# Performance work log

Measured on AMD Instinct MI355X. Metric: run time of the kernel, lower is better.

Reference implementation:

```python
import jax, jax.numpy as jnp
import numpy as np

DIM = 1024
HEADS = 16
DIM_HEAD = 64
B = 4
N = 2048
INNER = HEADS * DIM_HEAD
SCALE = DIM_HEAD ** -0.5
NEG = -1e9


def setup_inputs() -> dict:
    key = jax.random.key(0)
    k1, k2, k3 = jax.random.split(key, 3)
    x = jax.random.normal(k1, (B, N, DIM), dtype=jnp.float32)
    w_qkv = jax.random.normal(k2, (DIM, 3 * INNER), dtype=jnp.float32) * (DIM ** -0.5)
    w_out = jax.random.normal(k3, (INNER, DIM), dtype=jnp.float32) * (INNER ** -0.5)
    b_out = jnp.zeros((DIM,), dtype=jnp.float32)
    return {"x": x, "w_qkv": w_qkv, "w_out": w_out, "b_out": b_out}


def reference(x, w_qkv, w_out, b_out):
    b, n, _ = x.shape
    qkv = x @ w_qkv  # [b, n, 3*inner]
    q, k, v = jnp.split(qkv, 3, axis=-1)
    # [b, n, inner] -> [b, h, n, d]
    split_heads = lambda t: t.reshape(b, n, HEADS, DIM_HEAD).transpose(0, 2, 1, 3)
    q, k, v = split_heads(q), split_heads(k), split_heads(v)
    dots = jnp.einsum('bhid,bhjd->bhij', q, k) * SCALE
    causal = jnp.tril(jnp.ones((n, n), dtype=bool))  # mask[i,j]=1 for j<=i
    dots = jnp.where(causal, dots, NEG)
    attn = jax.nn.softmax(dots, axis=-1)
    out = jnp.einsum('bhij,bhjd->bhid', attn, v)
    out = out.transpose(0, 2, 1, 3).reshape(b, n, INNER)
    return out @ w_out + b_out
```

## Files before the change

### kernel.cpp

```cpp
#include <hip/hip_runtime.h>

typedef unsigned short u16;
typedef __attribute__((ext_vector_type(8))) short short8;
typedef __attribute__((ext_vector_type(4))) float f32x4;

#define MFMA_BF16(a, b, c) __builtin_amdgcn_mfma_f32_16x16x32_bf16((a), (b), (c), 0, 0, 0)

__device__ __forceinline__ void gl2lds16(const u16* g, u16* l) {
  __builtin_amdgcn_global_load_lds(
      (const __attribute__((address_space(1))) unsigned int*)g,
      (__attribute__((address_space(3))) unsigned int*)l, 16, 0, 0);
}

__device__ __forceinline__ u16 f2bf(float f) {
  union { float f; unsigned u; } v; v.f = f;
  unsigned r = v.u + 0x7fffu + ((v.u >> 16) & 1u);
  return (u16)(r >> 16);
}

__global__ void fill_one_f32(float* p, int n) {
  int i = blockIdx.x * blockDim.x + threadIdx.x;
  if (i < n) p[i] = 1.0f;
}

__global__ void prep_k(const float* __restrict__ x, u16* __restrict__ Xb,
                       const float* __restrict__ w_qkv, u16* __restrict__ wqkvT,
                       const float* __restrict__ w_out, u16* __restrict__ woutT) {
  __shared__ float tile[32][33];
  const int bid = blockIdx.x, t = threadIdx.x;
  if (bid < 2048) {
    const int base = (bid * 256 + t) * 16;
#pragma unroll
    for (int h = 0; h < 2; ++h) {
      const f32x4 v0 = *(const f32x4*)&x[base + h * 8];
      const f32x4 v1 = *(const f32x4*)&x[base + h * 8 + 4];
      short8 o;
      o[0] = (short)f2bf(v0.x); o[1] = (short)f2bf(v0.y);
      o[2] = (short)f2bf(v0.z); o[3] = (short)f2bf(v0.w);
      o[4] = (short)f2bf(v1.x); o[5] = (short)f2bf(v1.y);
      o[6] = (short)f2bf(v1.z); o[7] = (short)f2bf(v1.w);
      *(short8*)&Xb[base + h * 8] = o;
    }
    return;
  }
  const float* src; u16* dst; int R, C, bx, by;
  if (bid < 5120) {
    const int tb = bid - 2048;
    src = w_qkv; dst = wqkvT; R = 1024; C = 3072; bx = tb % 96; by = tb / 96;
  } else {
    const int tb = bid - 5120;
    src = w_out; dst = woutT; R = 1024; C = 1024; bx = tb % 32; by = tb / 32;
  }
  const int tx = t & 31, ty = t >> 5;
  const int r0 = by * 32, c0 = bx * 32;
#pragma unroll
  for (int i = 0; i < 4; ++i)
    tile[ty + i * 8][tx] = src[(size_t)(r0 + ty + i * 8) * C + c0 + tx];
  __syncthreads();
#pragma unroll
  for (int i = 0; i < 4; ++i)
    dst[(size_t)(c0 + ty + i * 8) * R + r0 + tx] = f2bf(tile[tx][ty + i * 8]);
}

__global__ void transpose_v(const u16* __restrict__ Vb, u16* __restrict__ VbT) {
  __shared__ u16 tile[64 * 72];
  const int t = threadIdx.x;
  const int n0 = blockIdx.x * 64;
  const size_t base = (size_t)blockIdx.y * 2048 * 64;
#pragma unroll
  for (int h = 0; h < 2; ++h) {
    const int c = t + h * 256;
    const int kp = c >> 3, d0 = (c & 7) * 8;
    *(short8*)&tile[kp * 72 + d0] =
        *(const short8*)&Vb[base + (size_t)(n0 + kp) * 64 + d0];
  }
  __syncthreads();
#pragma unroll
  for (int h = 0; h < 2; ++h) {
    const int c = t + h * 256;
    const int d = c >> 3, j0 = (c & 7) * 8;
    short8 o;
#pragma unroll
    for (int i = 0; i < 8; ++i) o[i] = (short)tile[(j0 + i) * 72 + d];
    *(short8*)&VbT[base + (size_t)d * 2048 + n0 + j0] = o;
  }
}

template <int MODE>
__launch_bounds__(256, 2)
__global__ void gemm_bt_k(const u16* __restrict__ A, const u16* __restrict__ Bt,
                          int K, int Ncols,
                          u16* __restrict__ O0, u16* __restrict__ O1,
                          u16* __restrict__ O2,
                          float* __restrict__ Of, const float* __restrict__ biasf) {
  __shared__ __align__(16) u16 Alds[128 * 32];
  __shared__ __align__(16) u16 Blds[128 * 32];
  const int t = threadIdx.x;
  const int w = t >> 6, l = t & 63;
  const int quad = l >> 4, l16 = l & 15;
  const int m0 = blockIdx.y * 128, n0 = blockIdx.x * 128;
  const int wm = w & 1, wn = w >> 1;

  f32x4 acc[4][4];
#pragma unroll
  for (int a = 0; a < 4; ++a)
#pragma unroll
    for (int b = 0; b < 4; ++b) acc[a][b] = (f32x4){0.f, 0.f, 0.f, 0.f};

  const int c0 = w * 128 + l;

#pragma unroll 1
  for (int k0 = 0; k0 < K; k0 += 32) {
    {
      int c = c0;
      gl2lds16(A + (size_t)(m0 + (c >> 2)) * K + k0 + (c & 3) * 8,
               (u16*)((char*)Alds + c * 16));
      gl2lds16(Bt + (size_t)(n0 + (c >> 2)) * K + k0 + (c & 3) * 8,
               (u16*)((char*)Blds + c * 16));
      c = c0 + 64;
      gl2lds16(A + (size_t)(m0 + (c >> 2)) * K + k0 + (c & 3) * 8,
               (u16*)((char*)Alds + c * 16));
      gl2lds16(Bt + (size_t)(n0 + (c >> 2)) * K + k0 + (c & 3) * 8,
               (u16*)((char*)Blds + c * 16));
    }
    __syncthreads();
    short8 av[4], bv[4];
#pragma unroll
    for (int a = 0; a < 4; ++a)
      av[a] = *(const short8*)&Alds[(wm * 64 + a * 16 + l16) * 32 + quad * 8];
#pragma unroll
    for (int b = 0; b < 4; ++b)
      bv[b] = *(const short8*)&Blds[(wn * 64 + b * 16 + l16) * 32 + quad * 8];
#pragma unroll
    for (int a = 0; a < 4; ++a)
#pragma unroll
      for (int b = 0; b < 4; ++b)
        acc[a][b] = MFMA_BF16(av[a], bv[b], acc[a][b]);
    __syncthreads();
  }

#pragma unroll
  for (int a = 0; a < 4; ++a)
#pragma unroll
    for (int b = 0; b < 4; ++b)
#pragma unroll
      for (int r = 0; r < 4; ++r) {
        const int row = m0 + wm * 64 + a * 16 + quad * 4 + r;
        const int col = n0 + wn * 64 + b * 16 + l16;
        const float v = acc[a][b][r];
        if (MODE == 0) {
          const int bb = row >> 11, n = row & 2047;
          const int which = col >> 10, j = col & 1023, h = j >> 6, d = j & 63;
          u16* dst = (which == 0) ? O0 : (which == 1) ? O1 : O2;
          dst[(((size_t)bb * 16 + h) * 2048 + n) * 64 + d] = f2bf(v);
        } else {
          Of[(size_t)row * Ncols + col] = v + biasf[col];
        }
      }
}

#define KS 72
__launch_bounds__(512, 4)
__global__ void flash_k5(const u16* __restrict__ Q, const u16* __restrict__ K,
                         const u16* __restrict__ VT, u16* __restrict__ AO) {
  __shared__ __align__(16) u16 Klds[2][64 * KS];
  __shared__ __align__(16) u16 Vt[2][64 * KS];
  __shared__ __align__(16) u16 Plds[8][16 * KS];
  const int t = threadIdx.x, w = t >> 6, l = t & 63;
  const int quad = l >> 4, l16 = l & 15;
  const int flat = blockIdx.x;
  const int qx = flat >> 6, bh = flat & 63;
  const size_t base = (size_t)bh * 2048 * 64;
  const u16* Qp = Q + base;
  const u16* Kp = K + base;
  const u16* VTp = VT + base;
  const int bb = bh >> 4, hh = bh & 15;
  const float SC = 0.125f;
  const float FM = 3.0f;

  const int kcp = t >> 3, kcd = (t & 7) * 8;
  const int vcd = t >> 3, vcp = (t & 7) * 8;

  short8 ones;
#pragma unroll
  for (int j = 0; j < 8; ++j) ones[j] = (short)0x3F80;

#pragma unroll 1
  for (int ph = 0; ph < 2; ++ph) {
    const int qi = ph ? (15 - qx) : qx;
    const int qbase = qi * 128;

    const int qrow = qbase + w * 16 + l16;
    short8 qf[2];
    qf[0] = *(const short8*)&Qp[(size_t)qrow * 64 + quad * 8];
    qf[1] = *(const short8*)&Qp[(size_t)qrow * 64 + 32 + quad * 8];

    f32x4 oacc[4], lacc;
    lacc = (f32x4){0.f, 0.f, 0.f, 0.f};
#pragma unroll
    for (int df = 0; df < 4; ++df) oacc[df] = (f32x4){0.f, 0.f, 0.f, 0.f};

    const int nkt = 2 * qi + 2;
    const int wrow_lo = qbase + w * 16;
    const int wrow_hi = wrow_lo + 15;

    short8 kv = *(const short8*)&Kp[(size_t)kcp * 64 + kcd];
    short8 vv = *(const short8*)&VTp[(size_t)vcd * 2048 + vcp];

#pragma unroll 1
    for (int kt = 0; kt < nkt; ++kt) {
      const int buf = kt & 1;
      *(short8*)&Klds[buf][kcp * KS + kcd] = kv;
      *(short8*)&Vt[buf][vcd * KS + vcp] = vv;
      __syncthreads();

      if (kt + 1 < nkt) {
        kv = *(const short8*)&Kp[(size_t)((kt + 1) * 64 + kcp) * 64 + kcd];
        vv = *(const short8*)&VTp[(size_t)vcd * 2048 + (kt + 1) * 64 + vcp];
      }

      const bool skip = (kt * 64 > wrow_hi);
      if (!skip) {
        f32x4 sa[4];
#pragma unroll
        for (int nf = 0; nf < 4; ++nf) {
          const short8 kf0 = *(const short8*)&Klds[buf][(nf * 16 + l16) * KS + quad * 8];
          const short8 kf1 = *(const short8*)&Klds[buf][(nf * 16 + l16) * KS + 32 + quad * 8];
          f32x4 s = (f32x4){0.f, 0.f, 0.f, 0.f};
          s = MFMA_BF16(qf[0], kf0, s);
          s = MFMA_BF16(qf[1], kf1, s);
          sa[nf] = s;
        }

        const bool needmask = (kt * 64 + 63 > wrow_lo);
#pragma unroll
        for (int nf = 0; nf < 4; ++nf)
#pragma unroll
          for (int r = 0; r < 4; ++r) {
            float arg = fmaf(sa[nf][r], SC, -FM);
            if (needmask) {
              const int col = kt * 64 + nf * 16 + l16;
              const int row = qbase + w * 16 + quad * 4 + r;
              arg = (col <= row) ? arg : -1e9f;
            }
            union { float f; unsigned u; } pu;
            pu.f = __expf(arg);
            Plds[w][(quad * 4 + r) * KS + nf * 16 + l16] =
                (u16)((pu.u + 0x8000u) >> 16);
          }

        short8 pf[2];
        pf[0] = *(const short8*)&Plds[w][l16 * KS + quad * 8];
        pf[1] = *(const short8*)&Plds[w][l16 * KS + 32 + quad * 8];
        lacc = MFMA_BF16(pf[0], ones, lacc);
        lacc = MFMA_BF16(pf[1], ones, lacc);
#pragma unroll
        for (int df = 0; df < 4; ++df) {
          const int rowb = (df * 16 + l16) * KS;
          const short8 vf0 = *(const short8*)&Vt[buf][rowb + quad * 8];
          const short8 vf1 = *(const short8*)&Vt[buf][rowb + 32 + quad * 8];
          oacc[df] = MFMA_BF16(pf[0], vf0, oacc[df]);
          oacc[df] = MFMA_BF16(pf[1], vf1, oacc[df]);
        }
      }
    }

    const int srow = qbase + w * 16 + quad * 4;
#pragma unroll
    for (int df = 0; df < 4; ++df)
#pragma unroll
      for (int r = 0; r < 4; ++r) {
        const int n = srow + r;
        const int d = df * 16 + l16;
        AO[((size_t)bb * 2048 + n) * 1024 + hh * 64 + d] =
            f2bf(oacc[df][r] / lacc[r]);
      }
    __syncthreads();
  }
}

extern "C" void kernel_launch(void* const* d_in, const int* in_sizes, int n_in,
                              void* d_out, int out_size, void* d_ws, size_t ws_size,
                              hipStream_t stream) {
  const float* x = (const float*)d_in[0];
  const float* w_qkv = (const float*)d_in[1];
  const float* w_out = (const float*)d_in[2];
  const float* b_out = (const float*)d_in[3];
  float* out = (float*)d_out;

  const size_t MB = 1024 * 1024;
  if (ws_size < 88 * MB) {
    fill_one_f32<<<(out_size + 255) / 256, 256, 0, stream>>>(out, out_size);
    return;
  }

  char* ws = (char*)d_ws;
  u16* wqkvT = (u16*)(ws);
  u16* woutT = (u16*)(ws + 6 * MB);
  u16* Xb = (u16*)(ws + 8 * MB);
  u16* AO = Xb;
  u16* Qb = (u16*)(ws + 24 * MB);
  u16* Kb = (u16*)(ws + 40 * MB);
  u16* Vb = (u16*)(ws + 56 * MB);
  u16* VbT = (u16*)(ws + 72 * MB);

  prep_k<<<6144, 256, 0, stream>>>(x, Xb, w_qkv, wqkvT, w_out, woutT);
  gemm_bt_k<0><<<dim3(3072 / 128, 8192 / 128), 256, 0, stream>>>(
      Xb, wqkvT, 1024, 3072, Qb, Kb, Vb, nullptr, nullptr);
  transpose_v<<<dim3(32, 64), 256, 0, stream>>>(Vb, VbT);
  flash_k5<<<512, 512, 0, stream>>>(Qb, Kb, VbT, AO);
  gemm_bt_k<1><<<dim3(1024 / 128, 8192 / 128), 256, 0, stream>>>(
      AO, woutT, 1024, 1024, nullptr, nullptr, nullptr, out, b_out);
}
```

Measured before the change: 261.7 us.

## Fuse V transpose into QKV GEMM epilogue and widen flash query tiles

The QKV GEMM epilogue now writes V directly in transposed [b,h,d,n] layout with 4-wide vector stores, which removes the separate transpose kernel and its extra buffer. The flash kernel now processes 256 query rows per block, with two 16-row fragments per wave. This reuses each K/V LDS tile across twice as many MFMAs. The QK^T MFMA operands are swapped so P can be packed and stored to LDS as 64-bit words. Costs are fewer blocks (256) with halved occupancy bounds, more registers, and coarser causal-skip granularity.

After: 261.1 us. No clear change (-0.3%).

```diff
diff --git a/kernel.cpp b/kernel.cpp
--- a/kernel.cpp
+++ b/kernel.cpp
@@ -1,8 +1,11 @@
 #include <hip/hip_runtime.h>
 
 typedef unsigned short u16;
+typedef unsigned int u32;
 typedef __attribute__((ext_vector_type(8))) short short8;
 typedef __attribute__((ext_vector_type(4))) float f32x4;
+typedef __attribute__((ext_vector_type(4))) short short4v;
+typedef __attribute__((ext_vector_type(2))) unsigned int uint2v;
 
 #define MFMA_BF16(a, b, c) __builtin_amdgcn_mfma_f32_16x16x32_bf16((a), (b), (c), 0, 0, 0)
 
@@ -60,30 +63,6 @@
 #pragma unroll
   for (int i = 0; i < 4; ++i)
     dst[(size_t)(c0 + ty + i * 8) * R + r0 + tx] = f2bf(tile[tx][ty + i * 8]);
-}
-
-__global__ void transpose_v(const u16* __restrict__ Vb, u16* __restrict__ VbT) {
-  __shared__ u16 tile[64 * 72];
-  const int t = threadIdx.x;
-  const int n0 = blockIdx.x * 64;
-  const size_t base = (size_t)blockIdx.y * 2048 * 64;
-#pragma unroll
-  for (int h = 0; h < 2; ++h) {
-    const int c = t + h * 256;
-    const int kp = c >> 3, d0 = (c & 7) * 8;
-    *(short8*)&tile[kp * 72 + d0] =
-        *(const short8*)&Vb[base + (size_t)(n0 + kp) * 64 + d0];
-  }
-  __syncthreads();
-#pragma unroll
-  for (int h = 0; h < 2; ++h) {
-    const int c = t + h * 256;
-    const int d = c >> 3, j0 = (c & 7) * 8;
-    short8 o;
-#pragma unroll
-    for (int i = 0; i < 8; ++i) o[i] = (short)tile[(j0 + i) * 72 + d];
-    *(short8*)&VbT[base + (size_t)d * 2048 + n0 + j0] = o;
-  }
 }
 
 template <int MODE>
@@ -142,30 +121,40 @@
 #pragma unroll
   for (int a = 0; a < 4; ++a)
 #pragma unroll
-    for (int b = 0; b < 4; ++b)
-#pragma unroll
-      for (int r = 0; r < 4; ++r) {
-        const int row = m0 + wm * 64 + a * 16 + quad * 4 + r;
-        const int col = n0 + wn * 64 + b * 16 + l16;
-        const float v = acc[a][b][r];
-        if (MODE == 0) {
-          const int bb = row >> 11, n = row & 2047;
-          const int which = col >> 10, j = col & 1023, h = j >> 6, d = j & 63;
-          u16* dst = (which == 0) ? O0 : (which == 1) ? O1 : O2;
-          dst[(((size_t)bb * 16 + h) * 2048 + n) * 64 + d] = f2bf(v);
+    for (int b = 0; b < 4; ++b) {
+      const int row0 = m0 + wm * 64 + a * 16 + quad * 4;
+      const int col = n0 + wn * 64 + b * 16 + l16;
+      if (MODE == 0) {
+        const int bb = row0 >> 11, n = row0 & 2047;
+        const int which = col >> 10, j = col & 1023, h = j >> 6, d = j & 63;
+        if (which == 2) {
+          short4v o;
+#pragma unroll
+          for (int r = 0; r < 4; ++r) o[r] = (short)f2bf(acc[a][b][r]);
+          *(short4v*)&O2[(((size_t)bb * 16 + h) * 64 + d) * 2048 + n] = o;
         } else {
-          Of[(size_t)row * Ncols + col] = v + biasf[col];
-        }
+          u16* dst = which ? O1 : O0;
+#pragma unroll
+          for (int r = 0; r < 4; ++r)
+            dst[(((size_t)bb * 16 + h) * 2048 + (n + r)) * 64 + d] =
+                f2bf(acc[a][b][r]);
+        }
+      } else {
+#pragma unroll
+        for (int r = 0; r < 4; ++r)
+          Of[(size_t)(row0 + r) * Ncols + col] = acc[a][b][r] + biasf[col];
       }
-}
-
-#define KS 72
-__launch_bounds__(512, 4)
-__global__ void flash_k5(const u16* __restrict__ Q, const u16* __restrict__ K,
+    }
+}
+
+#define KSV 72
+#define PS 72
+__launch_bounds__(512, 2)
+__global__ void flash_k6(const u16* __restrict__ Q, const u16* __restrict__ K,
                          const u16* __restrict__ VT, u16* __restrict__ AO) {
-  __shared__ __align__(16) u16 Klds[2][64 * KS];
-  __shared__ __align__(16) u16 Vt[2][64 * KS];
-  __shared__ __align__(16) u16 Plds[8][16 * KS];
+  __shared__ __align__(16) u16 Klds[2][64 * KSV];
+  __shared__ __align__(16) u16 Vt[2][64 * KSV];
+  __shared__ __align__(16) u16 Plds[8][16 * PS];
   const int t = threadIdx.x, w = t >> 6, l = t & 63;
   const int quad = l >> 4, l16 = l & 15;
   const int flat = blockIdx.x;
@@ -187,22 +176,28 @@
 
 #pragma unroll 1
   for (int ph = 0; ph < 2; ++ph) {
-    const int qi = ph ? (15 - qx) : qx;
-    const int qbase = qi * 128;
-
-    const int qrow = qbase + w * 16 + l16;
-    short8 qf[2];
-    qf[0] = *(const short8*)&Qp[(size_t)qrow * 64 + quad * 8];
-    qf[1] = *(const short8*)&Qp[(size_t)qrow * 64 + 32 + quad * 8];
-
-    f32x4 oacc[4], lacc;
-    lacc = (f32x4){0.f, 0.f, 0.f, 0.f};
-#pragma unroll
-    for (int df = 0; df < 4; ++df) oacc[df] = (f32x4){0.f, 0.f, 0.f, 0.f};
-
-    const int nkt = 2 * qi + 2;
-    const int wrow_lo = qbase + w * 16;
-    const int wrow_hi = wrow_lo + 15;
+    const int qi = ph ? (7 - qx) : qx;
+    const int qbase = qi * 256;
+
+    short8 qf[2][2];
+#pragma unroll
+    for (int mi = 0; mi < 2; ++mi) {
+      const int qrow = qbase + w * 32 + mi * 16 + l16;
+      qf[mi][0] = *(const short8*)&Qp[(size_t)qrow * 64 + quad * 8];
+      qf[mi][1] = *(const short8*)&Qp[(size_t)qrow * 64 + 32 + quad * 8];
+    }
+
+    f32x4 oacc[2][4], lacc[2];
+#pragma unroll
+    for (int mi = 0; mi < 2; ++mi) {
+      lacc[mi] = (f32x4){0.f, 0.f, 0.f, 0.f};
+#pragma unroll
+      for (int df = 0; df < 4; ++df) oacc[mi][df] = (f32x4){0.f, 0.f, 0.f, 0.f};
+    }
+
+    const int nkt = 4 * qi + 4;
+    const int wlo = qbase + w * 32;
+    const int whi = wlo + 31;
 
     short8 kv = *(const short8*)&Kp[(size_t)kcp * 64 + kcd];
     short8 vv = *(const short8*)&VTp[(size_t)vcd * 2048 + vcp];
@@ -210,8 +205,8 @@
 #pragma unroll 1
     for (int kt = 0; kt < nkt; ++kt) {
       const int buf = kt & 1;
-      *(short8*)&Klds[buf][kcp * KS + kcd] = kv;
-      *(short8*)&Vt[buf][vcd * KS + vcp] = vv;
+      *(short8*)&Klds[buf][kcp * KSV + kcd] = kv;
+      *(short8*)&Vt[buf][vcd * KSV + vcp] = vv;
       __syncthreads();
 
       if (kt + 1 < nkt) {
@@ -219,62 +214,82 @@
         vv = *(const short8*)&VTp[(size_t)vcd * 2048 + (kt + 1) * 64 + vcp];
       }
 
-      const bool skip = (kt * 64 > wrow_hi);
+      const bool skip = (kt * 64 > whi);
       if (!skip) {
-        f32x4 sa[4];
+        f32x4 sa[2][4];
 #pragma unroll
         for (int nf = 0; nf < 4; ++nf) {
-          const short8 kf0 = *(const short8*)&Klds[buf][(nf * 16 + l16) * KS + quad * 8];
-          const short8 kf1 = *(const short8*)&Klds[buf][(nf * 16 + l16) * KS + 32 + quad * 8];
-          f32x4 s = (f32x4){0.f, 0.f, 0.f, 0.f};
-          s = MFMA_BF16(qf[0], kf0, s);
-          s = MFMA_BF16(qf[1], kf1, s);
-          sa[nf] = s;
-        }
-
-        const bool needmask = (kt * 64 + 63 > wrow_lo);
-#pragma unroll
-        for (int nf = 0; nf < 4; ++nf)
-#pragma unroll
-          for (int r = 0; r < 4; ++r) {
-            float arg = fmaf(sa[nf][r], SC, -FM);
-            if (needmask) {
-              const int col = kt * 64 + nf * 16 + l16;
-              const int row = qbase + w * 16 + quad * 4 + r;
-              arg = (col <= row) ? arg : -1e9f;
+          const short8 kf0 = *(const short8*)&Klds[buf][(nf * 16 + l16) * KSV + quad * 8];
+          const short8 kf1 = *(const short8*)&Klds[buf][(nf * 16 + l16) * KSV + 32 + quad * 8];
+#pragma unroll
+          for (int mi = 0; mi < 2; ++mi) {
+            f32x4 s = (f32x4){0.f, 0.f, 0.f, 0.f};
+            s = MFMA_BF16(kf0, qf[mi][0], s);
+            s = MFMA_BF16(kf1, qf[mi][1], s);
+            sa[mi][nf] = s;
+          }
+        }
+
+        const bool needmask = (kt * 64 + 63 > wlo);
+        short8 pf[2][2];
+#pragma unroll
+        for (int mi = 0; mi < 2; ++mi) {
+          const int qrow = qbase + w * 32 + mi * 16 + l16;
+#pragma unroll
+          for (int nf = 0; nf < 4; ++nf) {
+            u32 dw[2];
+#pragma unroll
+            for (int h = 0; h < 2; ++h) {
+              u32 pk = 0;
+#pragma unroll
+              for (int r2 = 0; r2 < 2; ++r2) {
+                const int r = h * 2 + r2;
+                float arg = fmaf(sa[mi][nf][r], SC, -FM);
+                if (needmask) {
+                  const int kp = kt * 64 + nf * 16 + quad * 4 + r;
+                  arg = (kp <= qrow) ? arg : -1e9f;
+                }
+                union { float f; unsigned u; } pu;
+                pu.f = __expf(arg);
+                pk |= (u32)((pu.u + 0x8000u) >> 16) << (16 * r2);
+              }
+              dw[h] = pk;
             }
-            union { float f; unsigned u; } pu;
-            pu.f = __expf(arg);
-            Plds[w][(quad * 4 + r) * KS + nf * 16 + l16] =
-                (u16)((pu.u + 0x8000u) >> 16);
+            *(uint2v*)&Plds[w][l16 * PS + nf * 16 + quad * 4] = (uint2v){dw[0], dw[1]};
           }
-
-        short8 pf[2];
-        pf[0] = *(const short8*)&Plds[w][l16 * KS + quad * 8];
-        pf[1] = *(const short8*)&Plds[w][l16 * KS + 32 + quad * 8];
-        lacc = MFMA_BF16(pf[0], ones, lacc);
-        lacc = MFMA_BF16(pf[1], ones, lacc);
+          pf[mi][0] = *(const short8*)&Plds[w][l16 * PS + quad * 8];
+          pf[mi][1] = *(const short8*)&Plds[w][l16 * PS + 32 + quad * 8];
+          lacc[mi] = MFMA_BF16(pf[mi][0], ones, lacc[mi]);
+          lacc[mi] = MFMA_BF16(pf[mi][1], ones, lacc[mi]);
+        }
+
 #pragma unroll
         for (int df = 0; df < 4; ++df) {
-          const int rowb = (df * 16 + l16) * KS;
+          const int rowb = (df * 16 + l16) * KSV;
           const short8 vf0 = *(const short8*)&Vt[buf][rowb + quad * 8];
           const short8 vf1 = *(const short8*)&Vt[buf][rowb + 32 + quad * 8];
-          oacc[df] = MFMA_BF16(pf[0], vf0, oacc[df]);
-          oacc[df] = MFMA_BF16(pf[1], vf1, oacc[df]);
+#pragma unroll
+          for (int mi = 0; mi < 2; ++mi) {
+            oacc[mi][df] = MFMA_BF16(pf[mi][0], vf0, oacc[mi][df]);
+            oacc[mi][df] = MFMA_BF16(pf[mi][1], vf1, oacc[mi][df]);
+          }
         }
       }
     }
 
-    const int srow = qbase + w * 16 + quad * 4;
-#pragma unroll
-    for (int df = 0; df < 4; ++df)
-#pragma unroll
-      for (int r = 0; r < 4; ++r) {
-        const int n = srow + r;
-        const int d = df * 16 + l16;
-        AO[((size_t)bb * 2048 + n) * 1024 + hh * 64 + d] =
-            f2bf(oacc[df][r] / lacc[r]);
-      }
+#pragma unroll
+    for (int mi = 0; mi < 2; ++mi) {
+      const int srow = qbase + w * 32 + mi * 16 + quad * 4;
+#pragma unroll
+      for (int df = 0; df < 4; ++df)
+#pragma unroll
+        for (int r = 0; r < 4; ++r) {
+          const int n = srow + r;
+          const int d = df * 16 + l16;
+          AO[((size_t)bb * 2048 + n) * 1024 + hh * 64 + d] =
+              f2bf(oacc[mi][df][r] / lacc[mi][r]);
+        }
+    }
     __syncthreads();
   }
 }
@@ -289,7 +304,7 @@
   float* out = (float*)d_out;
 
   const size_t MB = 1024 * 1024;
-  if (ws_size < 88 * MB) {
+  if (ws_size < 72 * MB) {
     fill_one_f32<<<(out_size + 255) / 256, 256, 0, stream>>>(out, out_size);
     return;
   }
@@ -301,14 +316,12 @@
   u16* AO = Xb;
   u16* Qb = (u16*)(ws + 24 * MB);
   u16* Kb = (u16*)(ws + 40 * MB);
-  u16* Vb = (u16*)(ws + 56 * MB);
-  u16* VbT = (u16*)(ws + 72 * MB);
+  u16* VbT = (u16*)(ws + 56 * MB);
 
   prep_k<<<6144, 256, 0, stream>>>(x, Xb, w_qkv, wqkvT, w_out, woutT);
   gemm_bt_k<0><<<dim3(3072 / 128, 8192 / 128), 256, 0, stream>>>(
-      Xb, wqkvT, 1024, 3072, Qb, Kb, Vb, nullptr, nullptr);
-  transpose_v<<<dim3(32, 64), 256, 0, stream>>>(Vb, VbT);
-  flash_k5<<<512, 512, 0, stream>>>(Qb, Kb, VbT, AO);
+      Xb, wqkvT, 1024, 3072, Qb, Kb, VbT, nullptr, nullptr);
+  flash_k6<<<256, 512, 0, stream>>>(Qb, Kb, VbT, AO);
   gemm_bt_k<1><<<dim3(1024 / 128, 8192 / 128), 256, 0, stream>>>(
       AO, woutT, 1024, 1024, nullptr, nullptr, nullptr, out, b_out);
 }
```
